# Optimization experiments

Measured on AMD Instinct MI355X. Metric: run time of the kernel, lower is better.

Reference implementation:

```python
import jax, jax.numpy as jnp
import numpy as np

KH, KW = 3, 3
STRIDE = (1, 1)
PAD = 1


def _patches(x):
    # x: (B, C, H, W) -> (B, C, KH, KW, OH, OW)
    B, C, H, W = x.shape
    p = jax.lax.conv_general_dilated_patches(
        x, filter_shape=(KH, KW), window_strides=STRIDE,
        padding=[(PAD, PAD), (PAD, PAD)],
        dimension_numbers=('NCHW', 'OIHW', 'NCHW'))
    OH, OW = p.shape[2], p.shape[3]
    # feature dim of patches is ordered (C, KH, KW) — channel-major
    return p.reshape(B, C, KH, KW, OH, OW)


def setup_inputs() -> dict:
    key = jax.random.key(0)
    k1, k2 = jax.random.split(key, 2)
    B, C, H, W, O = 8, 32, 64, 64, 32
    OH = (H - KH + 2 * PAD) // STRIDE[0] + 1
    OW = (W - KW + 2 * PAD) // STRIDE[1] + 1
    x = jax.random.normal(k1, (B, C, H, W), dtype=jnp.float32)
    # xavier_uniform on the 6D weight (torch fan-in/out convention):
    recf = O * C * KH * KW
    fan_in, fan_out = OW * recf, OH * recf
    limit = float(np.sqrt(6.0 / (fan_in + fan_out)))
    weights = jax.random.uniform(k2, (OH, OW, O, C, KH, KW),
                                 minval=-limit, maxval=limit,
                                 dtype=jnp.float32)
    bias = jnp.zeros((O,), dtype=jnp.float32)
    return {"x": x, "weights": weights, "bias": bias}


def reference(x, weights, bias):
    # locally connected 2D conv: unique weight per output location.
    p = _patches(x)  # (B, C, KH, KW, OH, OW)
    # Faithful to the torch einsum 'bchw,ocwh->bo': the weight's kernel
    # spatial dims (kH,kW) are labeled (w,h), i.e. spatially transposed
    # relative to the patch.
    out = jnp.einsum('bchwij,ijocwh->boij', p, weights)
    return out + bias[None, :, None, None]
```

## Files before the change

### kernel.cpp

```cpp
#include <hip/hip_runtime.h>


#define NB 8
#define NC 32
#define NO 32
#define NH 64
#define NW 64
#define KK 288
#define K4 72
#define LOCS 8
#define XCOLS 10
#define NROWS (NB * NC * 3)
#define XNAT_SZ (NROWS * XCOLS)
#define XT_SZ (NB * KK)

__device__ __forceinline__ float reduce8(const float a[8], int kc) {
  float p8[8];
#pragma unroll
  for (int b = 0; b < 8; ++b) p8[b] = __shfl_xor(a[b], 4);
  float c4[4];
#pragma unroll
  for (int b = 0; b < 4; ++b)
    c4[b] = (kc & 4) ? (a[b + 4] + p8[b + 4]) : (a[b] + p8[b]);
  float p4[4];
#pragma unroll
  for (int b = 0; b < 4; ++b) p4[b] = __shfl_xor(c4[b], 2);
  float c2[2];
#pragma unroll
  for (int b = 0; b < 2; ++b)
    c2[b] = (kc & 2) ? (c4[b + 2] + p4[b + 2]) : (c4[b] + p4[b]);
  float p2[2];
#pragma unroll
  for (int b = 0; b < 2; ++b) p2[b] = __shfl_xor(c2[b], 1);
  return (kc & 1) ? (c2[1] + p2[1]) : (c2[0] + p2[0]);
}

__global__ __launch_bounds__(256) void lc2d_kernel(
    const float* __restrict__ x, const float* __restrict__ w,
    const float* __restrict__ bias, float* __restrict__ out) {
  const int g = blockIdx.x;
  const int loc0 = g * LOCS;
  const int i = loc0 >> 6;
  const int j0 = loc0 & 63;
  const int t = threadIdx.x;
  const int kc = t & 7;
  const int og = (t >> 3) & 15;
  const int bg = t >> 7;
  const int o0 = og * 2;
  const int b0 = bg * 4;
  const int o_out = o0 + (kc >> 2);
  const int b_out = b0 + (kc & 3);

  __shared__ float xnat[XNAT_SZ];
  __shared__ float xt[2][XT_SZ];
  __shared__ float obuf[LOCS][256];

  const float bia = bias[o_out];

#pragma unroll
  for (int it = 0; it < 30; ++it) {
    int e = t + it * 256;
    int row = e / XCOLS;
    int cc = e - row * XCOLS;
    int bc = row / 3;
    int yy = row - bc * 3;
    int y = i + yy - 1;
    int xc = j0 + cc - 1;
    float v = 0.f;
    if ((unsigned)y < 64u && (unsigned)xc < 64u)
      v = x[(bc * NH + y) * NW + xc];
    xnat[e] = v;
  }
  asm volatile("s_waitcnt lgkmcnt(0)\n\ts_barrier" ::: "memory");

  auto transpose = [&](int l, int buf) {
#pragma unroll
    for (int r = 0; r < 9; ++r) {
      int e = t + r * 256;
      int b = e / KK;
      int k = e - b * KK;
      int c = k / 9;
      int r9 = k - c * 9;
      int a = r9 / 3;
      int bb = r9 - a * 3;
      xt[buf][e] = xnat[((b * NC + c) * 3 + bb) * XCOLS + l + a];
    }
  };

  transpose(0, 0);

  float4 wreg[2][9];
  {
    const float4* p0 = reinterpret_cast<const float4*>(w) +
                       ((size_t)loc0 * NO + o0) * K4 + kc;
    const float4* p1 = p0 + K4;
#pragma unroll
    for (int s = 0; s < 9; ++s) { wreg[0][s] = p0[s * 8]; wreg[1][s] = p1[s * 8]; }
  }
  asm volatile("s_waitcnt lgkmcnt(0)\n\ts_barrier" ::: "memory");

#pragma unroll 1
  for (int l = 0; l < LOCS - 1; ++l) {
    const int cur = l & 1;
    transpose(l + 1, cur ^ 1);

    const float4* xt4 = reinterpret_cast<const float4*>(&xt[cur][0]);
    const float4* pn0 = reinterpret_cast<const float4*>(w) +
                        ((size_t)(loc0 + l + 1) * NO + o0) * K4 + kc;
    const float4* pn1 = pn0 + K4;

    float acc[2][4];
#pragma unroll
    for (int oi = 0; oi < 2; ++oi)
#pragma unroll
      for (int bi = 0; bi < 4; ++bi) acc[oi][bi] = 0.f;

#pragma unroll
    for (int s = 0; s < 9; ++s) {
      float4 w0 = wreg[0][s], w1 = wreg[1][s];
#pragma unroll
      for (int bi = 0; bi < 4; ++bi) {
        float4 xv = xt4[(b0 + bi) * K4 + s * 8 + kc];
        acc[0][bi] = fmaf(w0.x, xv.x, acc[0][bi]);
        acc[0][bi] = fmaf(w0.y, xv.y, acc[0][bi]);
        acc[0][bi] = fmaf(w0.z, xv.z, acc[0][bi]);
        acc[0][bi] = fmaf(w0.w, xv.w, acc[0][bi]);
        acc[1][bi] = fmaf(w1.x, xv.x, acc[1][bi]);
        acc[1][bi] = fmaf(w1.y, xv.y, acc[1][bi]);
        acc[1][bi] = fmaf(w1.z, xv.z, acc[1][bi]);
        acc[1][bi] = fmaf(w1.w, xv.w, acc[1][bi]);
      }
      wreg[0][s] = pn0[s * 8];
      wreg[1][s] = pn1[s * 8];
    }

    float a8[8];
#pragma unroll
    for (int oi = 0; oi < 2; ++oi)
#pragma unroll
      for (int bi = 0; bi < 4; ++bi) a8[oi * 4 + bi] = acc[oi][bi];
    obuf[l][t] = reduce8(a8, kc);
    asm volatile("s_waitcnt lgkmcnt(0)\n\ts_barrier" ::: "memory");
  }

  {
    const float4* xt4 =
        reinterpret_cast<const float4*>(&xt[(LOCS - 1) & 1][0]);
    float acc[2][4];
#pragma unroll
    for (int oi = 0; oi < 2; ++oi)
#pragma unroll
      for (int bi = 0; bi < 4; ++bi) acc[oi][bi] = 0.f;
#pragma unroll
    for (int s = 0; s < 9; ++s) {
      float4 w0 = wreg[0][s], w1 = wreg[1][s];
#pragma unroll
      for (int bi = 0; bi < 4; ++bi) {
        float4 xv = xt4[(b0 + bi) * K4 + s * 8 + kc];
        acc[0][bi] = fmaf(w0.x, xv.x, acc[0][bi]);
        acc[0][bi] = fmaf(w0.y, xv.y, acc[0][bi]);
        acc[0][bi] = fmaf(w0.z, xv.z, acc[0][bi]);
        acc[0][bi] = fmaf(w0.w, xv.w, acc[0][bi]);
        acc[1][bi] = fmaf(w1.x, xv.x, acc[1][bi]);
        acc[1][bi] = fmaf(w1.y, xv.y, acc[1][bi]);
        acc[1][bi] = fmaf(w1.z, xv.z, acc[1][bi]);
        acc[1][bi] = fmaf(w1.w, xv.w, acc[1][bi]);
      }
    }
    float a8[8];
#pragma unroll
    for (int oi = 0; oi < 2; ++oi)
#pragma unroll
      for (int bi = 0; bi < 4; ++bi) a8[oi * 4 + bi] = acc[oi][bi];
    obuf[LOCS - 1][t] = reduce8(a8, kc);
  }

  float4 fa, fb;
  fa.x = obuf[0][t] + bia; fa.y = obuf[1][t] + bia;
  fa.z = obuf[2][t] + bia; fa.w = obuf[3][t] + bia;
  fb.x = obuf[4][t] + bia; fb.y = obuf[5][t] + bia;
  fb.z = obuf[6][t] + bia; fb.w = obuf[7][t] + bia;
  float* op = &out[((b_out * NO + o_out) * NH + i) * NW + j0];
  *reinterpret_cast<float4*>(op) = fa;
  *reinterpret_cast<float4*>(op + 4) = fb;
}

extern "C" void kernel_launch(void* const* d_in, const int* in_sizes, int n_in,
                              void* d_out, int out_size, void* d_ws, size_t ws_size,
                              hipStream_t stream) {
  const float* x    = (const float*)d_in[0];
  const float* w    = (const float*)d_in[1];
  const float* bias = (const float*)d_in[2];
  float* out = (float*)d_out;
  lc2d_kernel<<<dim3(NH * NW / LOCS), dim3(256), 0, stream>>>(x, w, bias, out);
}
```

Baseline: 40.22 us.

## Halve locations per block, single-buffer transpose via registers, swizzle block order

```diff
diff --git a/kernel.cpp b/kernel.cpp
--- a/kernel.cpp
+++ b/kernel.cpp
@@ -8,8 +8,8 @@
 #define NW 64
 #define KK 288
 #define K4 72
-#define LOCS 8
-#define XCOLS 10
+#define LOCS 4
+#define XCOLS 6
 #define NROWS (NB * NC * 3)
 #define XNAT_SZ (NROWS * XCOLS)
 #define XT_SZ (NB * KK)
@@ -35,10 +35,11 @@
   return (kc & 1) ? (c2[1] + p2[1]) : (c2[0] + p2[0]);
 }
 
-__global__ __launch_bounds__(256) void lc2d_kernel(
+__global__ __launch_bounds__(256, 4) void lc2d_kernel(
     const float* __restrict__ x, const float* __restrict__ w,
     const float* __restrict__ bias, float* __restrict__ out) {
-  const int g = blockIdx.x;
+  const int bid = blockIdx.x;
+  const int g = (bid & 7) * 128 + (bid >> 3);
   const int loc0 = g * LOCS;
   const int i = loc0 >> 6;
   const int j0 = loc0 & 63;
@@ -51,14 +52,21 @@
   const int o_out = o0 + (kc >> 2);
   const int b_out = b0 + (kc & 3);
 
-  __shared__ float xnat[XNAT_SZ];
-  __shared__ float xt[2][XT_SZ];
-  __shared__ float obuf[LOCS][256];
+  __shared__ __align__(16) float xnat[XNAT_SZ];
+  __shared__ __align__(16) float xt[XT_SZ];
+  __shared__ __align__(16) float obuf[LOCS][256];
 
   const float bia = bias[o_out];
 
-#pragma unroll
-  for (int it = 0; it < 30; ++it) {
+  float4 wreg[2][9];
+  const float4* wb0 = reinterpret_cast<const float4*>(w) +
+                      ((size_t)loc0 * NO + o0) * K4 + kc;
+  const float4* wb1 = wb0 + K4;
+#pragma unroll
+  for (int s = 0; s < 9; ++s) { wreg[0][s] = wb0[s * 8]; wreg[1][s] = wb1[s * 8]; }
+
+#pragma unroll
+  for (int it = 0; it < 18; ++it) {
     int e = t + it * 256;
     int row = e / XCOLS;
     int cc = e - row * XCOLS;
@@ -73,7 +81,7 @@
   }
   asm volatile("s_waitcnt lgkmcnt(0)\n\ts_barrier" ::: "memory");
 
-  auto transpose = [&](int l, int buf) {
+  auto tr_read = [&](int l, float v[9]) {
 #pragma unroll
     for (int r = 0; r < 9; ++r) {
       int e = t + r * 256;
@@ -83,28 +91,25 @@
       int r9 = k - c * 9;
       int a = r9 / 3;
       int bb = r9 - a * 3;
-      xt[buf][e] = xnat[((b * NC + c) * 3 + bb) * XCOLS + l + a];
+      v[r] = xnat[((b * NC + c) * 3 + bb) * XCOLS + l + a];
     }
   };
 
-  transpose(0, 0);
-
-  float4 wreg[2][9];
   {
-    const float4* p0 = reinterpret_cast<const float4*>(w) +
-                       ((size_t)loc0 * NO + o0) * K4 + kc;
-    const float4* p1 = p0 + K4;
-#pragma unroll
-    for (int s = 0; s < 9; ++s) { wreg[0][s] = p0[s * 8]; wreg[1][s] = p1[s * 8]; }
+    float v0[9];
+    tr_read(0, v0);
+#pragma unroll
+    for (int r = 0; r < 9; ++r) xt[t + r * 256] = v0[r];
   }
   asm volatile("s_waitcnt lgkmcnt(0)\n\ts_barrier" ::: "memory");
+
+  const float4* xt4 = reinterpret_cast<const float4*>(xt);
 
 #pragma unroll 1
   for (int l = 0; l < LOCS - 1; ++l) {
-    const int cur = l & 1;
-    transpose(l + 1, cur ^ 1);
-
-    const float4* xt4 = reinterpret_cast<const float4*>(&xt[cur][0]);
+    float vnext[9];
+    tr_read(l + 1, vnext);
+
     const float4* pn0 = reinterpret_cast<const float4*>(w) +
                         ((size_t)(loc0 + l + 1) * NO + o0) * K4 + kc;
     const float4* pn1 = pn0 + K4;
@@ -140,12 +145,14 @@
 #pragma unroll
       for (int bi = 0; bi < 4; ++bi) a8[oi * 4 + bi] = acc[oi][bi];
     obuf[l][t] = reduce8(a8, kc);
+
+    asm volatile("s_barrier" ::: "memory");
+#pragma unroll
+    for (int r = 0; r < 9; ++r) xt[t + r * 256] = vnext[r];
     asm volatile("s_waitcnt lgkmcnt(0)\n\ts_barrier" ::: "memory");
   }
 
   {
-    const float4* xt4 =
-        reinterpret_cast<const float4*>(&xt[(LOCS - 1) & 1][0]);
     float acc[2][4];
 #pragma unroll
     for (int oi = 0; oi < 2; ++oi)
@@ -175,14 +182,12 @@
     obuf[LOCS - 1][t] = reduce8(a8, kc);
   }
 
-  float4 fa, fb;
-  fa.x = obuf[0][t] + bia; fa.y = obuf[1][t] + bia;
-  fa.z = obuf[2][t] + bia; fa.w = obuf[3][t] + bia;
-  fb.x = obuf[4][t] + bia; fb.y = obuf[5][t] + bia;
-  fb.z = obuf[6][t] + bia; fb.w = obuf[7][t] + bia;
-  float* op = &out[((b_out * NO + o_out) * NH + i) * NW + j0];
-  *reinterpret_cast<float4*>(op) = fa;
-  *reinterpret_cast<float4*>(op + 4) = fb;
+  float4 fa;
+  fa.x = obuf[0][t] + bia;
+  fa.y = obuf[1][t] + bia;
+  fa.z = obuf[2][t] + bia;
+  fa.w = obuf[3][t] + bia;
+  *reinterpret_cast<float4*>(&out[((b_out * NO + o_out) * NH + i) * NW + j0]) = fa;
 }
 
 extern "C" void kernel_launch(void* const* d_in, const int* in_sizes, int n_in,
```

New measurement: 34.13 us. 15.1% less time.
